# Performance work log

Measured on AMD Instinct MI355X. Metric: run time of the kernel, lower is better.

## Reference

```python
import jax, jax.numpy as jnp
import numpy as np
from jax import lax

EPS = 1e-8
ROUTINGS = 3


def squash(u, axis=-1):
    norm = jnp.linalg.norm(u, axis=axis, keepdims=True)
    scale = norm ** 2 / (1 + norm ** 2) / (norm + EPS)
    return scale * u


def conv2d(x, w, b, stride):
    y = lax.conv_general_dilated(x, w, window_strides=(stride, stride), padding='VALID',
                                 dimension_numbers=('NCHW', 'OIHW', 'NCHW'))
    return y + b[None, :, None, None]


def setup_inputs() -> dict:
    key = jax.random.key(0)
    ks = jax.random.split(key, 6)
    x = jax.random.normal(ks[0], (512, 1, 28, 28), dtype=jnp.float32)
    conv1_w = 0.1 * jax.random.normal(ks[1], (256, 1, 9, 9), dtype=jnp.float32)
    conv1_b = 0.1 * jax.random.normal(ks[2], (256,), dtype=jnp.float32)
    pc_w = 0.01 * jax.random.normal(ks[3], (256, 256, 9, 9), dtype=jnp.float32)
    pc_b = 0.01 * jax.random.normal(ks[4], (256,), dtype=jnp.float32)
    caps_w = 0.01 * jax.random.normal(ks[5], (10, 1152, 16, 8), dtype=jnp.float32)
    return {"x": x, "conv1_w": conv1_w, "conv1_b": conv1_b,
            "pc_w": pc_w, "pc_b": pc_b, "caps_w": caps_w}


def reference(x, conv1_w, conv1_b, pc_w, pc_b, caps_w):
    B = x.shape[0]
    # conv1 + relu: [B,1,28,28] -> [B,256,20,20]
    h = jax.nn.relu(conv2d(x, conv1_w, conv1_b, stride=1))
    # primary capsules: [B,256,20,20] -> [B,256,6,6] -> [B,1152,8], squash
    h = conv2d(h, pc_w, pc_b, stride=2)
    u = squash(h.reshape(B, 1152, 8))
    # votes: weight [O,I,Do,Di] x u [B,I,Di] -> x_hat [B,O,I,Do]
    x_hat = jnp.einsum('oidk,bik->boid', caps_w, u)
    x_hat_det = lax.stop_gradient(x_hat)
    b_logits = jnp.zeros((B, caps_w.shape[0], caps_w.shape[1]), dtype=x_hat.dtype)
    out_caps = None
    for i in range(ROUTINGS):
        c = jax.nn.softmax(b_logits, axis=1)  # softmax over output caps
        if i == ROUTINGS - 1:
            out_caps = squash(jnp.sum(c[..., None] * x_hat, axis=2))  # [B,O,Do]
        else:
            v = squash(jnp.sum(c[..., None] * x_hat_det, axis=2))  # [B,O,Do]
            b_logits = b_logits + jnp.einsum('bod,boid->boi', v, x_hat_det)
    length = jnp.linalg.norm(out_caps, axis=-1)  # [B,O]
    return length
```

## Files before the change

kernel.cpp:

```cpp
#include <hip/hip_runtime.h>
#include <hip/hip_bf16.h>
#include <hip/hip_fp16.h>
#include <math.h>

#define EPS 1e-8f

typedef __attribute__((ext_vector_type(8))) short bf16x8;
typedef __attribute__((ext_vector_type(8))) _Float16 f16x8;
typedef __attribute__((ext_vector_type(4))) float f32x4;
typedef __attribute__((ext_vector_type(16))) float f32x16;

__device__ static inline unsigned short f2bf(float f) {
    __hip_bfloat16 h = __float2bfloat16(f);
    return *reinterpret_cast<unsigned short*>(&h);
}
__device__ static inline unsigned short f2h(float f) {
    __half h = __float2half(f);
    return *reinterpret_cast<unsigned short*>(&h);
}

__device__ static inline void gld_lds16(const void* g, void* l) {
    __builtin_amdgcn_global_load_lds((const __attribute__((address_space(1))) void*)g,
                                     (__attribute__((address_space(3))) void*)l, 16, 0, 0);
}

__device__ static inline void h8tof(uint4 w, float* f) {
    float2 a = __half22float2(*(__half2*)&w.x);
    float2 b = __half22float2(*(__half2*)&w.y);
    float2 c = __half22float2(*(__half2*)&w.z);
    float2 d = __half22float2(*(__half2*)&w.w);
    f[0] = a.x; f[1] = a.y; f[2] = b.x; f[3] = b.y;
    f[4] = c.x; f[5] = c.y; f[6] = d.x; f[7] = d.y;
}

__global__ void k_prep(const float* __restrict__ x, unsigned short* __restrict__ xh,
                       const float* __restrict__ w1, unsigned short* __restrict__ wt1h,
                       const float* __restrict__ cw, __half* __restrict__ cwh) {
    int idx = blockIdx.x * 256 + threadIdx.x;
    if (idx < 401408) {
        xh[idx] = f2h(x[idx]);
    } else if (idx < 401408 + 24576) {
        int j = idx - 401408;
        int n = j / 96, k = j % 96;
        wt1h[j] = (k < 81) ? f2h(w1[n * 81 + k]) : (unsigned short)0;
    } else {
        int j = idx - 401408 - 24576;
        cwh[j] = __float2half(cw[j]);
    }
}

__global__ void k_tw2(const float* __restrict__ pw, unsigned short* __restrict__ wt2t) {
    int idx = blockIdx.x * 256 + threadIdx.x;
    int oc = idx / 20736, k = idx % 20736;
    int q = k >> 8, ic = k & 255;
    wt2t[idx] = f2bf(pw[oc * 20736 + ic * 81 + q]);
}

__global__ __launch_bounds__(256) void k_conv1(const unsigned short* __restrict__ xh,
                                               const unsigned short* __restrict__ wt1h,
                                               const float* __restrict__ b1,
                                               unsigned short* __restrict__ h1) {
    __shared__ unsigned short Asm[128 * 104];
    __shared__ unsigned short Bsm[128 * 104];
    const int tid = threadIdx.x;
    const int wave = tid >> 6, lane = tid & 63;
    const int ln15 = lane & 15, quad = lane >> 4;
    const int m0 = blockIdx.x * 128;
    const int n0 = blockIdx.y * 128;
    const int wm = (wave >> 1) * 64, wn = (wave & 1) * 64;

    for (int c = tid; c < 1536; c += 256) {
        int r = c / 12, ch = c % 12;
        uint4 v = *(const uint4*)(wt1h + (size_t)(n0 + r) * 96 + ch * 8);
        *(uint4*)(&Bsm[r * 104 + ch * 8]) = v;
    }
    for (int s = 0; s < 5; ++s) {
        int id = s * 256 + tid;
        if (id < 1152) {
            int m_l = id & 127, kh = id >> 7;
            int m = m0 + m_l;
            int b = m / 400, sp = m % 400;
            int oh = sp / 20, ow = sp % 20;
            const unsigned short* src = xh + b * 784 + (oh + kh) * 28 + ow;
            unsigned short* drow = &Asm[m_l * 104 + kh * 9];
#pragma unroll
            for (int w = 0; w < 9; ++w) drow[w] = src[w];
        }
    }
    for (int z = tid; z < 1920; z += 256) {
        int r = z / 15, kk = 81 + z % 15;
        Asm[r * 104 + kk] = 0;
    }
    __syncthreads();

    f32x4 acc[4][4];
#pragma unroll
    for (int i = 0; i < 4; ++i)
#pragma unroll
        for (int j = 0; j < 4; ++j) acc[i][j] = (f32x4)(0.f);

#pragma unroll
    for (int ks = 0; ks < 3; ++ks) {
        int k0 = (ks * 4 + quad) * 8;
        f16x8 af[4], bfr[4];
#pragma unroll
        for (int i = 0; i < 4; ++i)
            af[i] = *(const f16x8*)&Asm[(wm + i * 16 + ln15) * 104 + k0];
#pragma unroll
        for (int j = 0; j < 4; ++j)
            bfr[j] = *(const f16x8*)&Bsm[(wn + j * 16 + ln15) * 104 + k0];
#pragma unroll
        for (int i = 0; i < 4; ++i)
#pragma unroll
            for (int j = 0; j < 4; ++j)
                acc[i][j] = __builtin_amdgcn_mfma_f32_16x16x32_f16(
                    af[i], bfr[j], acc[i][j], 0, 0, 0);
    }

    float bias[4];
#pragma unroll
    for (int j = 0; j < 4; ++j) bias[j] = b1[n0 + wn + j * 16 + ln15];
#pragma unroll
    for (int i = 0; i < 4; ++i) {
#pragma unroll
        for (int r = 0; r < 4; ++r) {
            int m = m0 + wm + i * 16 + quad * 4 + r;
            unsigned short* dst = h1 + (size_t)m * 256 + n0 + wn;
#pragma unroll
            for (int j = 0; j < 4; ++j) {
                float v = acc[i][j][r] + bias[j];
                dst[j * 16 + ln15] = f2bf(v > 0.f ? v : 0.f);
            }
        }
    }
}

__global__ __launch_bounds__(256) void k_conv2(const unsigned short* __restrict__ h1,
                                               const unsigned short* __restrict__ wt2t,
                                               float* __restrict__ h2a) {
    __shared__ short Asm[128 * 64];
    __shared__ short Bsm[128 * 64];

    const int tid  = threadIdx.x;
    const int wave = tid >> 6, lane = tid & 63;
    const int ln31 = lane & 31, ln7 = lane & 7, khalf = lane >> 5;
    const int m0 = blockIdx.x * 128;
    const int n0 = blockIdx.y * 128;
    const int zz = blockIdx.z;
    const int kt0 = zz * 54;
    const int wm = (wave >> 1) * 64, wn = (wave & 1) * 64;

    const int rbase = wave * 32 + (lane >> 3);
    const int cswz8 = ((lane & 7) ^ ((lane >> 3) & 7)) * 8;

    size_t aptr[4];
    size_t bptr[4];
#pragma unroll
    for (int s = 0; s < 4; ++s) {
        int r = rbase + s * 8;
        int m = m0 + r;
        int b = m / 36, sp = m % 36;
        int oh = sp / 6, ow = sp % 6;
        aptr[s] = (size_t)((b * 20 + 2 * oh) * 20 + 2 * ow) * 256 + cswz8;
        bptr[s] = (size_t)(n0 + r) * 20736 + cswz8;
    }
    short* alds = &Asm[(wave * 32) * 64 + lane * 8];
    short* blds = &Bsm[(wave * 32) * 64 + lane * 8];

    f32x16 acc[2][2];
#pragma unroll
    for (int i = 0; i < 2; ++i)
#pragma unroll
        for (int j = 0; j < 2; ++j) acc[i][j] = (f32x16)(0.f);

    int q0 = kt0 >> 2;
    int kh = q0 / 9, kw = q0 - kh * 9;
    int pix = (kh * 20 + kw) * 256;

    for (int kt = kt0; kt < kt0 + 54; ++kt) {
        size_t aoff = (size_t)pix + ((kt & 3) << 6);
        size_t boff = (size_t)kt << 6;
#pragma unroll
        for (int s = 0; s < 4; ++s)
            gld_lds16(h1 + aptr[s] + aoff, alds + s * 512);
#pragma unroll
        for (int s = 0; s < 4; ++s)
            gld_lds16(wt2t + bptr[s] + boff, blds + s * 512);
        __syncthreads();
#pragma unroll
        for (int ks = 0; ks < 4; ++ks) {
            int slot = ((ks << 1) + khalf) ^ ln7;
            bf16x8 af[2], bfr[2];
#pragma unroll
            for (int i = 0; i < 2; ++i)
                af[i] = *(const bf16x8*)&Asm[(wm + i * 32 + ln31) * 64 + slot * 8];
#pragma unroll
            for (int j = 0; j < 2; ++j)
                bfr[j] = *(const bf16x8*)&Bsm[(wn + j * 32 + ln31) * 64 + slot * 8];
#pragma unroll
            for (int i = 0; i < 2; ++i)
#pragma unroll
                for (int j = 0; j < 2; ++j)
                    acc[i][j] = __builtin_amdgcn_mfma_f32_32x32x16_bf16(
                        af[i], bfr[j], acc[i][j], 0, 0, 0);
        }
        __syncthreads();
        if ((kt & 3) == 3) {
            if (kw == 8) { kw = 0; ++kh; pix += 12 * 256; }
            else         { ++kw;       pix += 256; }
        }
    }

    float* zs = h2a + (size_t)zz * 4718592;
#pragma unroll
    for (int i = 0; i < 2; ++i) {
#pragma unroll
        for (int j = 0; j < 2; ++j) {
#pragma unroll
            for (int reg = 0; reg < 16; ++reg) {
                int row = (reg & 3) + 8 * (reg >> 2) + 4 * khalf;
                int m = m0 + wm + i * 32 + row;
                zs[(size_t)m * 256 + n0 + wn + j * 32 + ln31] = acc[i][j][reg];
            }
        }
    }
}

__global__ __launch_bounds__(256) void k_squash(const float* __restrict__ h2a,
                                                const float* __restrict__ pb,
                                                unsigned short* __restrict__ u) {
    __shared__ float tile[36 * 260];
    const int tid = threadIdx.x;
    const int b = blockIdx.x;
    const float* base = h2a + (size_t)b * 36 * 256;
    for (int idx = tid; idx < 9216; idx += 256) {
        int sp = idx >> 8, c = idx & 255;
        float v = pb[c];
#pragma unroll
        for (int z = 0; z < 6; ++z) v += base[(size_t)z * 4718592 + sp * 256 + c];
        tile[sp * 260 + c] = v;
    }
    __syncthreads();
    for (int i2 = tid; i2 < 1152; i2 += 256) {
        int f0 = i2 * 8;
        float val[8];
        float n2 = 0.f;
#pragma unroll
        for (int e = 0; e < 8; ++e) {
            int f = f0 + e;
            int c = f / 36, sp = f - c * 36;
            val[e] = tile[sp * 260 + c];
            n2 += val[e] * val[e];
        }
        float n = sqrtf(n2);
        float s = n2 / (1.f + n2) / (n + EPS);
        unsigned short o8[8];
#pragma unroll
        for (int e = 0; e < 8; ++e) o8[e] = f2h(val[e] * s);
        *(uint4*)(u + (size_t)b * 9216 + f0) = *(uint4*)o8;
    }
}

__global__ __launch_bounds__(256) void k_xhat(const unsigned short* __restrict__ u,
                                              const __half* __restrict__ cwh,
                                              __half* __restrict__ xhat,
                                              float* __restrict__ s0) {
    __shared__ float ush[9216];
    __shared__ float part[4][16];
    const int b = blockIdx.x;
    const int t = threadIdx.x;
    const int wave = t >> 6;
    {
        const uint4* src = (const uint4*)(u + (size_t)b * 9216);
        for (int idx = t; idx < 1152; idx += 256) {
            uint4 v = src[idx];
            h8tof(v, &ush[idx * 8]);
        }
    }
    __syncthreads();

    for (int o = 0; o < 10; ++o) {
        float s_loc[16];
#pragma unroll
        for (int d = 0; d < 16; ++d) s_loc[d] = 0.f;
        for (int i = t; i < 1152; i += 256) {
            float ui[8];
            *(float4*)ui       = *(const float4*)&ush[i * 8];
            *(float4*)(ui + 4) = *(const float4*)&ush[i * 8 + 4];
            const uint4* wp = (const uint4*)(cwh + ((size_t)(o * 1152 + i) << 7));
            unsigned short xv[16];
#pragma unroll
            for (int d = 0; d < 16; ++d) {
                float f[8];
                h8tof(wp[d], f);
                float xh = f[0] * ui[0] + f[1] * ui[1] + f[2] * ui[2] + f[3] * ui[3]
                         + f[4] * ui[4] + f[5] * ui[5] + f[6] * ui[6] + f[7] * ui[7];
                s_loc[d] += xh;
                xv[d] = f2h(xh);
            }
            __half* dst = xhat + ((size_t)((b * 10 + o) * 1152 + i)) * 16;
            *(uint4*)dst       = *(uint4*)xv;
            *(uint4*)(dst + 8) = *(uint4*)(xv + 8);
        }
#pragma unroll
        for (int off = 32; off > 0; off >>= 1)
#pragma unroll
            for (int d = 0; d < 16; ++d) s_loc[d] += __shfl_down(s_loc[d], off, 64);
        if ((t & 63) == 0) {
#pragma unroll
            for (int d = 0; d < 16; ++d) part[wave][d] = s_loc[d];
        }
        __syncthreads();
        if (t < 16)
            s0[(b * 10 + o) * 16 + t] = part[0][t] + part[1][t] + part[2][t] + part[3][t];
        __syncthreads();
    }
}

__global__ __launch_bounds__(640) void k_routing(const __half* __restrict__ xhat,
                                                 const float* __restrict__ s0,
                                                 float* __restrict__ out) {
    __shared__ float dots[10][1152];
    __shared__ float sv[10][16];
    __shared__ float vsum[10][16];
    __shared__ float scale_sh[10];
    const int t = threadIdx.x;
    const int b = blockIdx.x;
    const int o = t >> 6, lane = t & 63;
    const __half* xb = xhat + ((size_t)(b * 10 + o) * 1152) * 16;

    if (t < 160) {
        int oo = t >> 4, d = t & 15;
        sv[oo][d] = 0.1f * s0[(b * 10 + oo) * 16 + d];
    }
    __syncthreads();
    if (t < 10) {
        float n2 = 0.f;
#pragma unroll
        for (int d = 0; d < 16; ++d) n2 += sv[t][d] * sv[t][d];
        float n = sqrtf(n2);
        scale_sh[t] = n2 / (1.f + n2) / (n + EPS);
    }
    __syncthreads();
    if (t < 160) vsum[t >> 4][t & 15] = sv[t >> 4][t & 15] * scale_sh[t >> 4];
    __syncthreads();

    for (int pass = 1; pass <= 2; ++pass) {
        float vs[16];
#pragma unroll
        for (int d = 0; d < 16; ++d) vs[d] = vsum[o][d];
        float s_loc[16];
#pragma unroll
        for (int d = 0; d < 16; ++d) s_loc[d] = 0.f;

        for (int g = 0; g < 6; ++g) {
            uint4 xq[3][2];
#pragma unroll
            for (int j = 0; j < 3; ++j) {
                int i = g * 192 + j * 64 + lane;
                const uint4* p = (const uint4*)(xb + (size_t)i * 16);
                xq[j][0] = p[0];
                xq[j][1] = p[1];
                float f0[8], f1[8];
                h8tof(xq[j][0], f0);
                h8tof(xq[j][1], f1);
                float dd = 0.f;
#pragma unroll
                for (int d = 0; d < 8; ++d) dd += vs[d] * f0[d] + vs[d + 8] * f1[d];
                dots[o][i] = dd;
            }
            __syncthreads();
            if (t < 192) {
                int i = g * 192 + t;
                float dv[10];
#pragma unroll
                for (int oo = 0; oo < 10; ++oo) dv[oo] = dots[oo][i];
                float mx = dv[0];
#pragma unroll
                for (int oo = 1; oo < 10; ++oo) mx = fmaxf(mx, dv[oo]);
                float se = 0.f;
#pragma unroll
                for (int oo = 0; oo < 10; ++oo) { dv[oo] = __expf(dv[oo] - mx); se += dv[oo]; }
                float si = 1.f / se;
#pragma unroll
                for (int oo = 0; oo < 10; ++oo) dots[oo][i] = dv[oo] * si;
            }
            __syncthreads();
#pragma unroll
            for (int j = 0; j < 3; ++j) {
                int i = g * 192 + j * 64 + lane;
                float c = dots[o][i];
                float f0[8], f1[8];
                h8tof(xq[j][0], f0);
                h8tof(xq[j][1], f1);
#pragma unroll
                for (int d = 0; d < 8; ++d) {
                    s_loc[d]     += c * f0[d];
                    s_loc[d + 8] += c * f1[d];
                }
            }
        }
#pragma unroll
        for (int off = 32; off > 0; off >>= 1)
#pragma unroll
            for (int d = 0; d < 16; ++d) s_loc[d] += __shfl_down(s_loc[d], off, 64);
        if (lane == 0) {
#pragma unroll
            for (int d = 0; d < 16; ++d) sv[o][d] = s_loc[d];
        }
        __syncthreads();
        if (pass == 1) {
            if (t < 10) {
                float n2 = 0.f;
#pragma unroll
                for (int d = 0; d < 16; ++d) n2 += sv[t][d] * sv[t][d];
                float n = sqrtf(n2);
                scale_sh[t] = n2 / (1.f + n2) / (n + EPS);
            }
            __syncthreads();
            if (t < 160) {
                int oo = t >> 4, d = t & 15;
                vsum[oo][d] += sv[oo][d] * scale_sh[oo];
            }
            __syncthreads();
        } else {
            if (t < 10) {
                float n2 = 0.f;
#pragma unroll
                for (int d = 0; d < 16; ++d) n2 += sv[t][d] * sv[t][d];
                float n = sqrtf(n2);
                out[b * 10 + t] = (n2 / (1.f + n2)) * (n / (n + EPS));
            }
        }
    }
}

extern "C" void kernel_launch(void* const* d_in, const int* in_sizes, int n_in,
                              void* d_out, int out_size, void* d_ws, size_t ws_size,
                              hipStream_t stream) {
    const float* x  = (const float*)d_in[0];
    const float* w1 = (const float*)d_in[1];
    const float* b1 = (const float*)d_in[2];
    const float* pw = (const float*)d_in[3];
    const float* pb = (const float*)d_in[4];
    const float* cw = (const float*)d_in[5];
    float* out = (float*)d_out;

    char* ws = (char*)d_ws;
    unsigned short* h1   = (unsigned short*)ws;
    float*          h2a  = (float*)(ws + 104857600);
    unsigned short* wt2t = (unsigned short*)(ws + 218103808);
    __half*         xhat = (__half*)ws;
    unsigned short* u    = (unsigned short*)(ws + 228720640);
    __half*         cwh  = (__half*)(ws + 238157824);
    unsigned short* xh16 = (unsigned short*)(ws + 241106944);
    unsigned short* wt1h = (unsigned short*)(ws + 241909760);
    float*          s0   = (float*)(ws + 241958912);

    k_prep<<<7424, 256, 0, stream>>>(x, xh16, w1, wt1h, cw, cwh);
    k_tw2<<<20736, 256, 0, stream>>>(pw, wt2t);
    k_conv1<<<dim3(1600, 2), 256, 0, stream>>>(xh16, wt1h, b1, h1);
    k_conv2<<<dim3(144, 2, 6), 256, 0, stream>>>(h1, wt2t, h2a);
    k_squash<<<512, 256, 0, stream>>>(h2a, pb, u);
    k_xhat<<<512, 256, 0, stream>>>(u, cwh, xhat, s0);
    k_routing<<<512, 640, 0, stream>>>(xhat, s0, out);
}
```

Measured before the change: 658.2 us.

## Load conv2 B operand directly to registers and transpose weights via LDS

The conv2 GEMM now loads the weight (B) fragments straight from global memory into registers per lane, dropping the B shared-memory tile and its LDS reads. The weight transpose kernel now stages each output channel through shared memory, so global reads and writes are coalesced instead of scattered. In exchange, B tiles are no longer shared through LDS, so each wave fetches its own slice and global/L2 traffic for weights rises. The per-iteration register load may also add latency before the MFMAs.

```diff
diff --git a/kernel.cpp b/kernel.cpp
--- a/kernel.cpp
+++ b/kernel.cpp
@@ -49,11 +49,24 @@
     }
 }
 
-__global__ void k_tw2(const float* __restrict__ pw, unsigned short* __restrict__ wt2t) {
-    int idx = blockIdx.x * 256 + threadIdx.x;
-    int oc = idx / 20736, k = idx % 20736;
-    int q = k >> 8, ic = k & 255;
-    wt2t[idx] = f2bf(pw[oc * 20736 + ic * 81 + q]);
+__global__ __launch_bounds__(256) void k_tw2(const float* __restrict__ pw,
+                                             unsigned short* __restrict__ wt2t) {
+    __shared__ unsigned short lds[20736];
+    const int oc = blockIdx.x, t = threadIdx.x;
+    const float* src = pw + (size_t)oc * 20736;
+#pragma unroll
+    for (int it = 0; it < 81; ++it) {
+        int j = it * 256 + t;
+        lds[j] = f2bf(src[j]);
+    }
+    __syncthreads();
+    unsigned short* dst = wt2t + (size_t)oc * 20736;
+#pragma unroll
+    for (int it = 0; it < 81; ++it) {
+        int j = it * 256 + t;
+        int q = j >> 8, ic = j & 255;
+        dst[j] = lds[ic * 81 + q];
+    }
 }
 
 __global__ __launch_bounds__(256) void k_conv1(const unsigned short* __restrict__ xh,
@@ -139,7 +152,6 @@
                                                const unsigned short* __restrict__ wt2t,
                                                float* __restrict__ h2a) {
     __shared__ short Asm[128 * 64];
-    __shared__ short Bsm[128 * 64];
 
     const int tid  = threadIdx.x;
     const int wave = tid >> 6, lane = tid & 63;
@@ -154,7 +166,6 @@
     const int cswz8 = ((lane & 7) ^ ((lane >> 3) & 7)) * 8;
 
     size_t aptr[4];
-    size_t bptr[4];
 #pragma unroll
     for (int s = 0; s < 4; ++s) {
         int r = rbase + s * 8;
@@ -162,10 +173,13 @@
         int b = m / 36, sp = m % 36;
         int oh = sp / 6, ow = sp % 6;
         aptr[s] = (size_t)((b * 20 + 2 * oh) * 20 + 2 * ow) * 256 + cswz8;
-        bptr[s] = (size_t)(n0 + r) * 20736 + cswz8;
     }
     short* alds = &Asm[(wave * 32) * 64 + lane * 8];
-    short* blds = &Bsm[(wave * 32) * 64 + lane * 8];
+
+    size_t brow[2];
+#pragma unroll
+    for (int j = 0; j < 2; ++j)
+        brow[j] = (size_t)(n0 + wn + j * 32 + ln31) * 20736 + khalf * 8;
 
     f32x16 acc[2][2];
 #pragma unroll
@@ -179,30 +193,29 @@
 
     for (int kt = kt0; kt < kt0 + 54; ++kt) {
         size_t aoff = (size_t)pix + ((kt & 3) << 6);
-        size_t boff = (size_t)kt << 6;
 #pragma unroll
         for (int s = 0; s < 4; ++s)
             gld_lds16(h1 + aptr[s] + aoff, alds + s * 512);
-#pragma unroll
-        for (int s = 0; s < 4; ++s)
-            gld_lds16(wt2t + bptr[s] + boff, blds + s * 512);
+        uint4 breg[4][2];
+#pragma unroll
+        for (int ks = 0; ks < 4; ++ks)
+#pragma unroll
+            for (int j = 0; j < 2; ++j)
+                breg[ks][j] = *(const uint4*)(wt2t + brow[j] + (size_t)kt * 64 + ks * 16);
         __syncthreads();
 #pragma unroll
         for (int ks = 0; ks < 4; ++ks) {
             int slot = ((ks << 1) + khalf) ^ ln7;
-            bf16x8 af[2], bfr[2];
+            bf16x8 af[2];
 #pragma unroll
             for (int i = 0; i < 2; ++i)
                 af[i] = *(const bf16x8*)&Asm[(wm + i * 32 + ln31) * 64 + slot * 8];
 #pragma unroll
-            for (int j = 0; j < 2; ++j)
-                bfr[j] = *(const bf16x8*)&Bsm[(wn + j * 32 + ln31) * 64 + slot * 8];
-#pragma unroll
             for (int i = 0; i < 2; ++i)
 #pragma unroll
                 for (int j = 0; j < 2; ++j)
                     acc[i][j] = __builtin_amdgcn_mfma_f32_32x32x16_bf16(
-                        af[i], bfr[j], acc[i][j], 0, 0, 0);
+                        af[i], *(const bf16x8*)&breg[ks][j], acc[i][j], 0, 0, 0);
         }
         __syncthreads();
         if ((kt & 3) == 3) {
@@ -458,7 +471,7 @@
     float*          s0   = (float*)(ws + 241958912);
 
     k_prep<<<7424, 256, 0, stream>>>(x, xh16, w1, wt1h, cw, cwh);
-    k_tw2<<<20736, 256, 0, stream>>>(pw, wt2t);
+    k_tw2<<<256, 256, 0, stream>>>(pw, wt2t);
     k_conv1<<<dim3(1600, 2), 256, 0, stream>>>(xh16, wt1h, b1, h1);
     k_conv2<<<dim3(144, 2, 6), 256, 0, stream>>>(h1, wt2t, h2a);
     k_squash<<<512, 256, 0, stream>>>(h2a, pb, u);
```

New measurement: 831.9 us. 1.26x slower.
